# Performance work log

Measured on AMD Instinct MI355X. Metric: run time of the kernel, lower is better.

The kernel has to match this reference:

```python
import jax, jax.numpy as jnp
import numpy as np

NEG_BIG = -1e9  # matches masked_fill value -1000000000.0


def setup_inputs() -> dict:
    key = jax.random.key(0)
    k1, k2, k3, k4 = jax.random.split(key, 4)
    B, H, S, D = 2, 16, 2048, 64
    q = jax.random.normal(k1, (B, H, S, D), dtype=jnp.float32)
    k = jax.random.normal(k2, (B, H, S, D), dtype=jnp.float32)
    v = jax.random.normal(k3, (B, H, S, D), dtype=jnp.float32)
    mask = jax.random.randint(k4, (B, 1, S, S), 0, 2).astype(bool)
    return {"q": q, "k": k, "v": v, "mask": mask}


def reference(q, k, v, mask):
    d_k = q.shape[-1]
    scale = 1.0 / jnp.sqrt(jnp.float32(d_k))
    # scores: [B,H,S,S]
    scores = jnp.einsum("bhqd,bhkd->bhqk", q, k) * scale
    scores = jnp.where(mask, NEG_BIG, scores)
    atten = jax.nn.softmax(scores, axis=-1)
    # dropout p=0.0 (eval) -> identity
    out = jnp.einsum("bhqk,bhkd->bhqd", atten, v)
    return (out, atten)
```

## Files before the change

kernel.cpp:

```cpp
#include <hip/hip_runtime.h>

#define S 2048
#define D 64
#define BH 32
#define CHUNK 128
#define NCH (S / CHUNK)
#define MTILE 64

typedef __attribute__((ext_vector_type(8))) short bfrag;
typedef __attribute__((ext_vector_type(4))) float f32x4;
typedef __attribute__((ext_vector_type(2))) unsigned int u32x2;
typedef __attribute__((ext_vector_type(8))) unsigned short u16x8;

__device__ __forceinline__ unsigned short f2bf(float f) {
    unsigned int u = __builtin_bit_cast(unsigned int, f);
    u += 0x7fffu + ((u >> 16) & 1u);
    return (unsigned short)(u >> 16);
}
__device__ __forceinline__ ushort4 f2bf4(float4 f) {
    ushort4 u;
    u.x = f2bf(f.x); u.y = f2bf(f.y); u.z = f2bf(f.z); u.w = f2bf(f.w);
    return u;
}
__device__ __forceinline__ void gl_lds16(const void* g, void* l) {
    __builtin_amdgcn_global_load_lds(
        (const __attribute__((address_space(1))) unsigned int*)g,
        (__attribute__((address_space(3))) unsigned int*)l, 16, 0, 0);
}


__global__ void mask_detect_kernel(const unsigned int* __restrict__ m, int* __restrict__ flag) {
    __shared__ int any;
    if (threadIdx.x == 0) any = 0;
    __syncthreads();
    unsigned int v0 = m[threadIdx.x];
    unsigned int v1 = m[threadIdx.x + 256];
    unsigned int v2 = m[threadIdx.x + 512];
    unsigned int v3 = m[threadIdx.x + 768];
    if (v0 > 1u || v1 > 1u || v2 > 1u || v3 > 1u) any = 1;
    __syncthreads();
    if (threadIdx.x == 0) *flag = any;
}

__global__ void conv_k_kernel(const float* __restrict__ k, unsigned short* __restrict__ kbf) {
    const size_t i8 = ((size_t)blockIdx.x * 256 + threadIdx.x) * 8;
    float4 a = *(const float4*)&k[i8];
    float4 b = *(const float4*)&k[i8 + 4];
    union { u16x8 v; ushort4 h[2]; } u;
    u.h[0] = f2bf4(a); u.h[1] = f2bf4(b);
    *(u16x8*)&kbf[i8] = u.v;
}

__global__ void v_transpose_kernel(const float* __restrict__ v, unsigned short* __restrict__ vtbf) {
    __shared__ unsigned short Ts[64][72];
    const int t = threadIdx.x;
    const int bh = blockIdx.x >> 5;
    const int k0 = (blockIdx.x & 31) * 64;
    {
        const int kr = t >> 2, c0 = (t & 3) * 16;
        const float* src = &v[((size_t)bh * S + k0 + kr) * D + c0];
#pragma unroll
        for (int i = 0; i < 4; ++i) {
            float4 f = *(const float4*)&src[i * 4];
            *(ushort4*)&Ts[kr][c0 + i * 4] = f2bf4(f);
        }
    }
    __syncthreads();
    {
        const int d = t >> 2, kq = (t & 3) * 16;
        union { u16x8 v8; unsigned short e[8]; } u0, u1;
#pragma unroll
        for (int i = 0; i < 8; ++i) u0.e[i] = Ts[kq + i][d];
#pragma unroll
        for (int i = 0; i < 8; ++i) u1.e[i] = Ts[kq + 8 + i][d];
        unsigned short* dst = &vtbf[(size_t)bh * D * S + (size_t)d * S + k0 + kq];
        *(u16x8*)&dst[0] = u0.v8;
        *(u16x8*)&dst[8] = u1.v8;
    }
}

__global__ void mask_pack_kernel(const int* __restrict__ mi, const unsigned char* __restrict__ mb,
                                 const int* __restrict__ flag, unsigned int* __restrict__ mbits) {
    const int idx = blockIdx.x * 256 + threadIdx.x;
    const int row = idx >> 6, w = idx & 63;
    unsigned bits = 0;
    if (*flag) {
        const unsigned char* src = &mb[(size_t)row * S + w * 32];
#pragma unroll
        for (int i = 0; i < 8; ++i) {
            unsigned u = *(const unsigned int*)&src[i * 4] & 0x01010101u;
            unsigned nib = (u | (u >> 7) | (u >> 14) | (u >> 21)) & 0xFu;
            bits |= nib << (i * 4);
        }
    } else {
        const int* src = &mi[(size_t)row * S + w * 32];
#pragma unroll
        for (int i = 0; i < 8; ++i) {
            int4 v = *(const int4*)&src[i * 4];
            unsigned nib = (unsigned)(v.x & 1) | ((unsigned)(v.y & 1) << 1) |
                           ((unsigned)(v.z & 1) << 2) | ((unsigned)(v.w & 1) << 3);
            bits |= nib << (i * 4);
        }
    }
    mbits[idx] = bits;
}


__global__ __launch_bounds__(256, 2)
void attn_mfma_kernel(const float* __restrict__ q,
                      const unsigned short* __restrict__ kbf,
                      const unsigned short* __restrict__ vtbf,
                      const unsigned int* __restrict__ mbits,
                      float* __restrict__ out, float* __restrict__ atten) {
    __shared__ __attribute__((aligned(16))) unsigned short smem[40960];
    const int KB[2] = {0, 8192};
    const int VB[2] = {16384, 24576};
    const int PB = 32768;

    const int t    = threadIdx.x;
    const int lane = t & 63;
    const int wv   = t >> 6;
    const int quad = lane >> 4;
    const int l16  = lane & 15;
    const int bh   = blockIdx.y;
    const int r0   = blockIdx.x * MTILE;
    const int bz   = bh >> 4;

    const unsigned short* kbh = kbf + (size_t)bh * S * D;
    const unsigned short* vbh = vtbf + (size_t)bh * S * D;
    const unsigned int*   mrowp = mbits + ((size_t)bz * S + r0 + wv * 16 + l16) * 64;

    int kdst[4], ksrc[4], vdst[4], vsrc[4];
#pragma unroll
    for (int i = 0; i < 4; ++i) {
        const int off = wv * 4096 + i * 1024 + lane * 16;
        {
            const int r = off >> 7, cch = (off >> 4) & 7, c = cch ^ (r & 7);
            kdst[i] = off >> 1;
            ksrc[i] = r * 64 + c * 8;
        }
        {
            const int d = off >> 8, p = (off >> 4) & 15, c = p ^ (d & 7);
            vdst[i] = off >> 1;
            vsrc[i] = d * S + c * 8;
        }
    }

    bfrag qf[2];
    {
        const float* qrow = q + ((size_t)bh * S + r0 + wv * 16 + l16) * D + quad * 8;
#pragma unroll
        for (int ks = 0; ks < 2; ++ks) {
            float4 a = *(const float4*)&qrow[ks * 32];
            float4 b = *(const float4*)&qrow[ks * 32 + 4];
            a.x *= 0.125f; a.y *= 0.125f; a.z *= 0.125f; a.w *= 0.125f;
            b.x *= 0.125f; b.y *= 0.125f; b.z *= 0.125f; b.w *= 0.125f;
            union { bfrag f; ushort4 h[2]; } u;
            u.h[0] = f2bf4(a);
            u.h[1] = f2bf4(b);
            qf[ks] = u.f;
        }
    }

    float lsum = 0.f;
    f32x4 acc_o[4];
#pragma unroll
    for (int n = 0; n < 4; ++n) acc_o[n] = (f32x4){0.f, 0.f, 0.f, 0.f};

    unsigned short* Pme = &smem[PB + wv * 2048];

#pragma unroll
    for (int i = 0; i < 4; ++i) {
        gl_lds16(&kbh[ksrc[i]], &smem[KB[0] + kdst[i]]);
        gl_lds16(&vbh[vsrc[i]], &smem[VB[0] + vdst[i]]);
    }

    for (int ch = 0; ch < NCH; ++ch) {
        const int b = ch & 1;
        __syncthreads();

        if (ch + 1 < NCH) {
            const int j1 = (ch + 1) * CHUNK;
#pragma unroll
            for (int i = 0; i < 4; ++i) {
                gl_lds16(&kbh[j1 * 64 + ksrc[i]], &smem[KB[b ^ 1] + kdst[i]]);
                gl_lds16(&vbh[j1 + vsrc[i]], &smem[VB[b ^ 1] + vdst[i]]);
            }
        }
        const uint4 mm = *(const uint4*)(mrowp + ch * 4);

        const unsigned short* Kb = &smem[KB[b]];
        f32x4 sacc[8];
#pragma unroll
        for (int nt = 0; nt < 8; ++nt) sacc[nt] = (f32x4){0.f, 0.f, 0.f, 0.f};
#pragma unroll
        for (int ks = 0; ks < 2; ++ks) {
#pragma unroll
            for (int nt = 0; nt < 8; ++nt) {
                bfrag kf = *(const bfrag*)&Kb[(nt * 16 + l16) * 64 +
                                              (((ks * 4 + quad) ^ (l16 & 7)) * 8)];
                sacc[nt] = __builtin_amdgcn_mfma_f32_16x16x32_bf16(kf, qf[ks], sacc[nt], 0, 0, 0);
            }
        }

        unsigned mw[4] = {mm.x >> (quad * 4), mm.y >> (quad * 4),
                          mm.z >> (quad * 4), mm.w >> (quad * 4)};

#pragma unroll
        for (int nt = 0; nt < 8; ++nt) {
            float p[4];
#pragma unroll
            for (int rg = 0; rg < 4; ++rg) {
                const unsigned bit = (mw[nt >> 1] >> (((nt & 1) << 4) + rg)) & 1u;
                p[rg] = bit ? 0.f : __expf(sacc[nt][rg]);
                lsum += p[rg];
            }
            unsigned w0 = (unsigned)f2bf(p[0]) | ((unsigned)f2bf(p[1]) << 16);
            unsigned w1 = (unsigned)f2bf(p[2]) | ((unsigned)f2bf(p[3]) << 16);
            const int cch = (2 * nt + (quad >> 1)) ^ (l16 & 7);
            *(u32x2*)&Pme[l16 * 128 + cch * 8 + (quad & 1) * 4] = (u32x2){w0, w1};
        }

        const unsigned short* Vb = &smem[VB[b]];
#pragma unroll
        for (int ks = 0; ks < 4; ++ks) {
            bfrag ap = *(const bfrag*)&Pme[l16 * 128 + (((4 * ks + quad) ^ (l16 & 7)) * 8)];
#pragma unroll
            for (int nt = 0; nt < 4; ++nt) {
                bfrag bv2 = *(const bfrag*)&Vb[(nt * 16 + l16) * 128 +
                                               (((ks * 4 + quad) ^ (l16 & 7)) * 8)];
                acc_o[nt] = __builtin_amdgcn_mfma_f32_16x16x32_bf16(ap, bv2, acc_o[nt], 0, 0, 0);
            }
        }
    }

    float s2 = lsum;
    s2 += __shfl_xor(s2, 16);
    s2 += __shfl_xor(s2, 32);
    const float linv_self = 1.f / s2;
    float lv[4];
#pragma unroll
    for (int rg = 0; rg < 4; ++rg) lv[rg] = __shfl(linv_self, quad * 4 + rg);

#pragma unroll
    for (int i = 0; i < 4; ++i)
        gl_lds16(&kbh[ksrc[i]], &smem[KB[0] + kdst[i]]);

#pragma unroll
    for (int nt = 0; nt < 4; ++nt) {
#pragma unroll
        for (int rg = 0; rg < 4; ++rg) {
            const int row = r0 + wv * 16 + quad * 4 + rg;
            out[((size_t)bh * S + row) * D + nt * 16 + l16] = acc_o[nt][rg] * lv[rg];
        }
    }

    float* Twv = reinterpret_cast<float*>(&smem[VB[0]]) + wv * 2048;
    for (int ch = 0; ch < NCH; ++ch) {
        const int b = ch & 1;
        const int j0 = ch * CHUNK;
        __syncthreads();

        if (ch + 1 < NCH) {
            const int j1 = (ch + 1) * CHUNK;
#pragma unroll
            for (int i = 0; i < 4; ++i)
                gl_lds16(&kbh[j1 * 64 + ksrc[i]], &smem[KB[b ^ 1] + kdst[i]]);
        }
        const uint4 mm = *(const uint4*)(mrowp + ch * 4);

        const unsigned short* Kb = &smem[KB[b]];
        f32x4 sacc[8];
#pragma unroll
        for (int nt = 0; nt < 8; ++nt) sacc[nt] = (f32x4){0.f, 0.f, 0.f, 0.f};
#pragma unroll
        for (int ks = 0; ks < 2; ++ks) {
#pragma unroll
            for (int nt = 0; nt < 8; ++nt) {
                bfrag kf = *(const bfrag*)&Kb[(nt * 16 + l16) * 64 +
                                              (((ks * 4 + quad) ^ (l16 & 7)) * 8)];
                sacc[nt] = __builtin_amdgcn_mfma_f32_16x16x32_bf16(kf, qf[ks], sacc[nt], 0, 0, 0);
            }
        }

        unsigned mw[4] = {mm.x >> (quad * 4), mm.y >> (quad * 4),
                          mm.z >> (quad * 4), mm.w >> (quad * 4)};

#pragma unroll
        for (int nt = 0; nt < 8; ++nt) {
            f32x4 vals;
#pragma unroll
            for (int rg = 0; rg < 4; ++rg) {
                const unsigned bit = (mw[nt >> 1] >> (((nt & 1) << 4) + rg)) & 1u;
                vals[rg] = bit ? 0.f : __expf(sacc[nt][rg]) * linv_self;
            }
            *(f32x4*)&Twv[l16 * 128 + (((nt * 4 + quad) ^ (l16 & 7)) * 4)] = vals;
        }

#pragma unroll
        for (int rr = 0; rr < 4; ++rr) {
            const int row = rr * 4 + quad;
#pragma unroll
            for (int h = 0; h < 2; ++h) {
                const f32x4 vals = *(const f32x4*)&Twv[row * 128 +
                                                       (((h * 16 + l16) ^ (row & 7)) * 4)];
                __builtin_nontemporal_store(
                    vals, (f32x4*)&atten[((size_t)bh * S + r0 + wv * 16 + row) * S +
                                         j0 + h * 64 + l16 * 4]);
            }
        }
    }
}

extern "C" void kernel_launch(void* const* d_in, const int* in_sizes, int n_in,
                              void* d_out, int out_size, void* d_ws, size_t ws_size,
                              hipStream_t stream) {
    const float* q = (const float*)d_in[0];
    const float* k = (const float*)d_in[1];
    const float* v = (const float*)d_in[2];
    const void* mask = d_in[3];
    float* out   = (float*)d_out;
    float* atten = out + (size_t)BH * S * D;

    char* ws = (char*)d_ws;
    int* flag = (int*)ws;
    unsigned short* kbf  = (unsigned short*)(ws + 256);
    unsigned short* vtbf = kbf + (size_t)BH * S * D;
    unsigned int*   mbits = (unsigned int*)(vtbf + (size_t)BH * S * D);

    mask_detect_kernel<<<1, 256, 0, stream>>>((const unsigned int*)mask, flag);
    conv_k_kernel<<<2048, 256, 0, stream>>>(k, kbf);
    v_transpose_kernel<<<1024, 256, 0, stream>>>(v, vtbf);
    mask_pack_kernel<<<1024, 256, 0, stream>>>((const int*)mask, (const unsigned char*)mask,
                                               flag, mbits);

    dim3 grid(S / MTILE, BH);
    attn_mfma_kernel<<<grid, 256, 0, stream>>>(q, kbf, vtbf, mbits, out, atten);
}
```

Before: 663.0 us.

## Split attention into separate output and attention-write kernels with remapped block order

Splits the fused attention kernel into two launches. Phase A computes the output and the per-row softmax normalizer, which it stores to workspace. Phase B recomputes the scores, reading K directly from global memory into registers, and writes the attention matrix with higher occupancy. Q is pre-converted to bf16 alongside K, and blocks are remapped so that groups of heads with the same row tile are scheduled together for better cache reuse. The cost is an extra launch, a small workspace round trip, and K reads in phase B that go uncached through LDS.

```diff
diff --git a/kernel.cpp b/kernel.cpp
--- a/kernel.cpp
+++ b/kernel.cpp
@@ -26,6 +26,12 @@
     __builtin_amdgcn_global_load_lds(
         (const __attribute__((address_space(1))) unsigned int*)g,
         (__attribute__((address_space(3))) unsigned int*)l, 16, 0, 0);
+}
+
+__device__ __forceinline__ void decode_block(int w, int& bh, int& r0) {
+    const int r = w & 7, bx = (w >> 3) & 31, g = w >> 8;
+    bh = g * 8 + r;
+    r0 = bx * MTILE;
 }
 
 
@@ -42,13 +48,25 @@
     if (threadIdx.x == 0) *flag = any;
 }
 
-__global__ void conv_k_kernel(const float* __restrict__ k, unsigned short* __restrict__ kbf) {
+__global__ void conv_qk_kernel(const float* __restrict__ q, const float* __restrict__ k,
+                               unsigned short* __restrict__ qbf, unsigned short* __restrict__ kbf) {
     const size_t i8 = ((size_t)blockIdx.x * 256 + threadIdx.x) * 8;
-    float4 a = *(const float4*)&k[i8];
-    float4 b = *(const float4*)&k[i8 + 4];
-    union { u16x8 v; ushort4 h[2]; } u;
-    u.h[0] = f2bf4(a); u.h[1] = f2bf4(b);
-    *(u16x8*)&kbf[i8] = u.v;
+    {
+        float4 a = *(const float4*)&q[i8];
+        float4 b = *(const float4*)&q[i8 + 4];
+        a.x *= 0.125f; a.y *= 0.125f; a.z *= 0.125f; a.w *= 0.125f;
+        b.x *= 0.125f; b.y *= 0.125f; b.z *= 0.125f; b.w *= 0.125f;
+        union { u16x8 v; ushort4 h[2]; } u;
+        u.h[0] = f2bf4(a); u.h[1] = f2bf4(b);
+        *(u16x8*)&qbf[i8] = u.v;
+    }
+    {
+        float4 a = *(const float4*)&k[i8];
+        float4 b = *(const float4*)&k[i8 + 4];
+        union { u16x8 v; ushort4 h[2]; } u;
+        u.h[0] = f2bf4(a); u.h[1] = f2bf4(b);
+        *(u16x8*)&kbf[i8] = u.v;
+    }
 }
 
 __global__ void v_transpose_kernel(const float* __restrict__ v, unsigned short* __restrict__ vtbf) {
@@ -107,11 +125,11 @@
 
 
 __global__ __launch_bounds__(256, 2)
-void attn_mfma_kernel(const float* __restrict__ q,
-                      const unsigned short* __restrict__ kbf,
-                      const unsigned short* __restrict__ vtbf,
-                      const unsigned int* __restrict__ mbits,
-                      float* __restrict__ out, float* __restrict__ atten) {
+void attn_phaseA(const unsigned short* __restrict__ qbf,
+                 const unsigned short* __restrict__ kbf,
+                 const unsigned short* __restrict__ vtbf,
+                 const unsigned int* __restrict__ mbits,
+                 float* __restrict__ out, float* __restrict__ linv_ws) {
     __shared__ __attribute__((aligned(16))) unsigned short smem[40960];
     const int KB[2] = {0, 8192};
     const int VB[2] = {16384, 24576};
@@ -122,9 +140,9 @@
     const int wv   = t >> 6;
     const int quad = lane >> 4;
     const int l16  = lane & 15;
-    const int bh   = blockIdx.y;
-    const int r0   = blockIdx.x * MTILE;
-    const int bz   = bh >> 4;
+    int bh, r0;
+    decode_block(blockIdx.x, bh, r0);
+    const int bz = bh >> 4;
 
     const unsigned short* kbh = kbf + (size_t)bh * S * D;
     const unsigned short* vbh = vtbf + (size_t)bh * S * D;
@@ -148,18 +166,9 @@
 
     bfrag qf[2];
     {
-        const float* qrow = q + ((size_t)bh * S + r0 + wv * 16 + l16) * D + quad * 8;
-#pragma unroll
-        for (int ks = 0; ks < 2; ++ks) {
-            float4 a = *(const float4*)&qrow[ks * 32];
-            float4 b = *(const float4*)&qrow[ks * 32 + 4];
-            a.x *= 0.125f; a.y *= 0.125f; a.z *= 0.125f; a.w *= 0.125f;
-            b.x *= 0.125f; b.y *= 0.125f; b.z *= 0.125f; b.w *= 0.125f;
-            union { bfrag f; ushort4 h[2]; } u;
-            u.h[0] = f2bf4(a);
-            u.h[1] = f2bf4(b);
-            qf[ks] = u.f;
-        }
+        const unsigned short* qrow = qbf + ((size_t)bh * S + r0 + wv * 16 + l16) * D;
+        qf[0] = *(const bfrag*)&qrow[quad * 8];
+        qf[1] = *(const bfrag*)&qrow[32 + quad * 8];
     }
 
     float lsum = 0.f;
@@ -238,13 +247,10 @@
     s2 += __shfl_xor(s2, 16);
     s2 += __shfl_xor(s2, 32);
     const float linv_self = 1.f / s2;
+    if (quad == 0) linv_ws[(size_t)bh * S + r0 + wv * 16 + l16] = linv_self;
     float lv[4];
 #pragma unroll
     for (int rg = 0; rg < 4; ++rg) lv[rg] = __shfl(linv_self, quad * 4 + rg);
-
-#pragma unroll
-    for (int i = 0; i < 4; ++i)
-        gl_lds16(&kbh[ksrc[i]], &smem[KB[0] + kdst[i]]);
 
 #pragma unroll
     for (int nt = 0; nt < 4; ++nt) {
@@ -254,34 +260,60 @@
             out[((size_t)bh * S + row) * D + nt * 16 + l16] = acc_o[nt][rg] * lv[rg];
         }
     }
-
-    float* Twv = reinterpret_cast<float*>(&smem[VB[0]]) + wv * 2048;
+}
+
+
+__global__ __launch_bounds__(256, 3)
+void attn_phaseB(const unsigned short* __restrict__ qbf,
+                 const unsigned short* __restrict__ kbf,
+                 const unsigned int* __restrict__ mbits,
+                 const float* __restrict__ linv_ws,
+                 float* __restrict__ atten) {
+    __shared__ __attribute__((aligned(16))) float Tw[4][2048];
+
+    const int t    = threadIdx.x;
+    const int lane = t & 63;
+    const int wv   = t >> 6;
+    const int quad = lane >> 4;
+    const int l16  = lane & 15;
+    int bh, r0;
+    decode_block(blockIdx.x, bh, r0);
+    const int bz = bh >> 4;
+
+    const unsigned short* kbh = kbf + (size_t)bh * S * D;
+    const unsigned int*   mrowp = mbits + ((size_t)bz * S + r0 + wv * 16 + l16) * 64;
+    const float linv_self = linv_ws[(size_t)bh * S + r0 + wv * 16 + l16];
+
+    bfrag qf[2];
+    {
+        const unsigned short* qrow = qbf + ((size_t)bh * S + r0 + wv * 16 + l16) * D;
+        qf[0] = *(const bfrag*)&qrow[quad * 8];
+        qf[1] = *(const bfrag*)&qrow[32 + quad * 8];
+    }
+
+    float* Twv = Tw[wv];
+
     for (int ch = 0; ch < NCH; ++ch) {
-        const int b = ch & 1;
         const int j0 = ch * CHUNK;
-        __syncthreads();
-
-        if (ch + 1 < NCH) {
-            const int j1 = (ch + 1) * CHUNK;
-#pragma unroll
-            for (int i = 0; i < 4; ++i)
-                gl_lds16(&kbh[j1 * 64 + ksrc[i]], &smem[KB[b ^ 1] + kdst[i]]);
-        }
         const uint4 mm = *(const uint4*)(mrowp + ch * 4);
 
-        const unsigned short* Kb = &smem[KB[b]];
+        bfrag kf[2][8];
+#pragma unroll
+        for (int ks = 0; ks < 2; ++ks)
+#pragma unroll
+            for (int nt = 0; nt < 8; ++nt)
+                kf[ks][nt] = *(const bfrag*)&kbh[(size_t)(j0 + nt * 16 + l16) * D +
+                                                 ks * 32 + quad * 8];
+
         f32x4 sacc[8];
 #pragma unroll
         for (int nt = 0; nt < 8; ++nt) sacc[nt] = (f32x4){0.f, 0.f, 0.f, 0.f};
 #pragma unroll
-        for (int ks = 0; ks < 2; ++ks) {
-#pragma unroll
-            for (int nt = 0; nt < 8; ++nt) {
-                bfrag kf = *(const bfrag*)&Kb[(nt * 16 + l16) * 64 +
-                                              (((ks * 4 + quad) ^ (l16 & 7)) * 8)];
-                sacc[nt] = __builtin_amdgcn_mfma_f32_16x16x32_bf16(kf, qf[ks], sacc[nt], 0, 0, 0);
-            }
-        }
+        for (int ks = 0; ks < 2; ++ks)
+#pragma unroll
+            for (int nt = 0; nt < 8; ++nt)
+                sacc[nt] = __builtin_amdgcn_mfma_f32_16x16x32_bf16(kf[ks][nt], qf[ks],
+                                                                   sacc[nt], 0, 0, 0);
 
         unsigned mw[4] = {mm.x >> (quad * 4), mm.y >> (quad * 4),
                           mm.z >> (quad * 4), mm.w >> (quad * 4)};
@@ -324,16 +356,18 @@
 
     char* ws = (char*)d_ws;
     int* flag = (int*)ws;
-    unsigned short* kbf  = (unsigned short*)(ws + 256);
+    unsigned short* qbf  = (unsigned short*)(ws + 256);
+    unsigned short* kbf  = qbf + (size_t)BH * S * D;
     unsigned short* vtbf = kbf + (size_t)BH * S * D;
     unsigned int*   mbits = (unsigned int*)(vtbf + (size_t)BH * S * D);
+    float*          linv_ws = (float*)(mbits + (size_t)2 * S * (S / 32));
 
     mask_detect_kernel<<<1, 256, 0, stream>>>((const unsigned int*)mask, flag);
-    conv_k_kernel<<<2048, 256, 0, stream>>>(k, kbf);
+    conv_qk_kernel<<<2048, 256, 0, stream>>>(q, k, qbf, kbf);
     v_transpose_kernel<<<1024, 256, 0, stream>>>(v, vtbf);
     mask_pack_kernel<<<1024, 256, 0, stream>>>((const int*)mask, (const unsigned char*)mask,
                                                flag, mbits);
 
-    dim3 grid(S / MTILE, BH);
-    attn_mfma_kernel<<<grid, 256, 0, stream>>>(q, kbf, vtbf, mbits, out, atten);
-}
+    attn_phaseA<<<1024, 256, 0, stream>>>(qbf, kbf, vtbf, mbits, out, linv_ws);
+    attn_phaseB<<<1024, 256, 0, stream>>>(qbf, kbf, mbits, linv_ws, atten);
+}
```

After: 724.7 us. 1.09x slower.

## Preconvert Q to bf16, remap block order across heads, nontemporal output stores

Applied to the files above, without the earlier changes.

Q is scaled and converted to bf16 in the same prep kernel that converts K, so the attention kernel loads ready bf16 fragments. The grid becomes 1D, with a decode that interleaves 8 heads per group so concurrently running blocks share the same batch's mask rows and K/V data in L2. Output stores use nontemporal hints to avoid polluting the cache. The changes add a bf16 Q buffer in the workspace and one more pass over Q in the prep kernel.

```diff
diff --git a/kernel.cpp b/kernel.cpp
--- a/kernel.cpp
+++ b/kernel.cpp
@@ -26,6 +26,12 @@
     __builtin_amdgcn_global_load_lds(
         (const __attribute__((address_space(1))) unsigned int*)g,
         (__attribute__((address_space(3))) unsigned int*)l, 16, 0, 0);
+}
+
+__device__ __forceinline__ void decode_block(int w, int& bh, int& r0) {
+    const int r = w & 7, bx = (w >> 3) & 31, g = w >> 8;
+    bh = g * 8 + r;
+    r0 = bx * MTILE;
 }
 
 
@@ -42,13 +48,25 @@
     if (threadIdx.x == 0) *flag = any;
 }
 
-__global__ void conv_k_kernel(const float* __restrict__ k, unsigned short* __restrict__ kbf) {
+__global__ void conv_qk_kernel(const float* __restrict__ q, const float* __restrict__ k,
+                               unsigned short* __restrict__ qbf, unsigned short* __restrict__ kbf) {
     const size_t i8 = ((size_t)blockIdx.x * 256 + threadIdx.x) * 8;
-    float4 a = *(const float4*)&k[i8];
-    float4 b = *(const float4*)&k[i8 + 4];
-    union { u16x8 v; ushort4 h[2]; } u;
-    u.h[0] = f2bf4(a); u.h[1] = f2bf4(b);
-    *(u16x8*)&kbf[i8] = u.v;
+    {
+        float4 a = *(const float4*)&q[i8];
+        float4 b = *(const float4*)&q[i8 + 4];
+        a.x *= 0.125f; a.y *= 0.125f; a.z *= 0.125f; a.w *= 0.125f;
+        b.x *= 0.125f; b.y *= 0.125f; b.z *= 0.125f; b.w *= 0.125f;
+        union { u16x8 v; ushort4 h[2]; } u;
+        u.h[0] = f2bf4(a); u.h[1] = f2bf4(b);
+        *(u16x8*)&qbf[i8] = u.v;
+    }
+    {
+        float4 a = *(const float4*)&k[i8];
+        float4 b = *(const float4*)&k[i8 + 4];
+        union { u16x8 v; ushort4 h[2]; } u;
+        u.h[0] = f2bf4(a); u.h[1] = f2bf4(b);
+        *(u16x8*)&kbf[i8] = u.v;
+    }
 }
 
 __global__ void v_transpose_kernel(const float* __restrict__ v, unsigned short* __restrict__ vtbf) {
@@ -107,7 +125,7 @@
 
 
 __global__ __launch_bounds__(256, 2)
-void attn_mfma_kernel(const float* __restrict__ q,
+void attn_mfma_kernel(const unsigned short* __restrict__ qbf,
                       const unsigned short* __restrict__ kbf,
                       const unsigned short* __restrict__ vtbf,
                       const unsigned int* __restrict__ mbits,
@@ -122,9 +140,9 @@
     const int wv   = t >> 6;
     const int quad = lane >> 4;
     const int l16  = lane & 15;
-    const int bh   = blockIdx.y;
-    const int r0   = blockIdx.x * MTILE;
-    const int bz   = bh >> 4;
+    int bh, r0;
+    decode_block(blockIdx.x, bh, r0);
+    const int bz = bh >> 4;
 
     const unsigned short* kbh = kbf + (size_t)bh * S * D;
     const unsigned short* vbh = vtbf + (size_t)bh * S * D;
@@ -148,18 +166,9 @@
 
     bfrag qf[2];
     {
-        const float* qrow = q + ((size_t)bh * S + r0 + wv * 16 + l16) * D + quad * 8;
-#pragma unroll
-        for (int ks = 0; ks < 2; ++ks) {
-            float4 a = *(const float4*)&qrow[ks * 32];
-            float4 b = *(const float4*)&qrow[ks * 32 + 4];
-            a.x *= 0.125f; a.y *= 0.125f; a.z *= 0.125f; a.w *= 0.125f;
-            b.x *= 0.125f; b.y *= 0.125f; b.z *= 0.125f; b.w *= 0.125f;
-            union { bfrag f; ushort4 h[2]; } u;
-            u.h[0] = f2bf4(a);
-            u.h[1] = f2bf4(b);
-            qf[ks] = u.f;
-        }
+        const unsigned short* qrow = qbf + ((size_t)bh * S + r0 + wv * 16 + l16) * D;
+        qf[0] = *(const bfrag*)&qrow[quad * 8];
+        qf[1] = *(const bfrag*)&qrow[32 + quad * 8];
     }
 
     float lsum = 0.f;
@@ -251,7 +260,9 @@
 #pragma unroll
         for (int rg = 0; rg < 4; ++rg) {
             const int row = r0 + wv * 16 + quad * 4 + rg;
-            out[((size_t)bh * S + row) * D + nt * 16 + l16] = acc_o[nt][rg] * lv[rg];
+            __builtin_nontemporal_store(
+                acc_o[nt][rg] * lv[rg],
+                &out[((size_t)bh * S + row) * D + nt * 16 + l16]);
         }
     }
 
@@ -324,16 +335,16 @@
 
     char* ws = (char*)d_ws;
     int* flag = (int*)ws;
-    unsigned short* kbf  = (unsigned short*)(ws + 256);
+    unsigned short* qbf  = (unsigned short*)(ws + 256);
+    unsigned short* kbf  = qbf + (size_t)BH * S * D;
     unsigned short* vtbf = kbf + (size_t)BH * S * D;
     unsigned int*   mbits = (unsigned int*)(vtbf + (size_t)BH * S * D);
 
     mask_detect_kernel<<<1, 256, 0, stream>>>((const unsigned int*)mask, flag);
-    conv_k_kernel<<<2048, 256, 0, stream>>>(k, kbf);
+    conv_qk_kernel<<<2048, 256, 0, stream>>>(q, k, qbf, kbf);
     v_transpose_kernel<<<1024, 256, 0, stream>>>(v, vtbf);
     mask_pack_kernel<<<1024, 256, 0, stream>>>((const int*)mask, (const unsigned char*)mask,
                                                flag, mbits);
 
-    dim3 grid(S / MTILE, BH);
-    attn_mfma_kernel<<<grid, 256, 0, stream>>>(q, kbf, vtbf, mbits, out, atten);
-}
+    attn_mfma_kernel<<<1024, 256, 0, stream>>>(qbf, kbf, vtbf, mbits, out, atten);
+}
```

New measurement: 658.6 us. About the same (-0.7%).
